# Kernel tuning notes

Measured on AMD Instinct MI355X. Metric: run time of the kernel, lower is better.

Reference implementation:

```python
import jax, jax.numpy as jnp
import numpy as np

N_NODES = 100000
N_EDGES = 3200000
D_IN = 256
D_OUT = 128


def setup_inputs() -> dict:
    key = jax.random.key(0)
    k1, k2, k3, k4, k5 = jax.random.split(key, 5)
    x = jax.random.normal(k1, (N_NODES, D_IN), dtype=jnp.float32)
    edge_src = jax.random.randint(k2, (N_EDGES,), 0, N_NODES, dtype=jnp.int32)
    edge_dst = jax.random.randint(k3, (N_EDGES,), 0, N_NODES, dtype=jnp.int32)
    edge_weight = jax.random.uniform(k4, (N_EDGES,), dtype=jnp.float32)
    # GraphConvolution weight init: uniform(-stdv, stdv), stdv = 1/sqrt(in+out)
    stdv = 1.0 / np.sqrt(D_IN + D_OUT)
    W = jax.random.uniform(k5, (D_IN, D_OUT), dtype=jnp.float32,
                           minval=-stdv, maxval=stdv)
    return {"x": x, "edge_src": edge_src, "edge_dst": edge_dst,
            "edge_weight": edge_weight, "W": W}


def reference(x, edge_src, edge_dst, edge_weight, W):
    # support = input @ weight  (dense GEMM)  [N, D_OUT]
    support = x @ W
    # out = spmm(adj, support): out[d] = sum_{e: dst(e)=d} w_e * support[src(e)]
    msgs = support[edge_src] * edge_weight[:, None]       # [E, D_OUT] gather
    out = jax.ops.segment_sum(msgs, edge_dst, num_segments=N_NODES)  # scatter-add
    return out
```

## Files before the change

### kernel.cpp

```cpp
#include <hip/hip_runtime.h>


#define DIN 256
#define DOUT 128
#define SB_SHIFT 10
#define SB_NODES 1024
#define MAX_NSB 128
#define TILE 4096
#define SPLIT 2

__device__ __forceinline__ unsigned pack_bf16x2(float a, float b) {
  unsigned ua = __float_as_uint(a);
  unsigned ub = __float_as_uint(b);
  ua += 0x7fffu + ((ua >> 16) & 1u);
  ub += 0x7fffu + ((ub >> 16) & 1u);
  return (ua >> 16) | (ub & 0xffff0000u);
}
__device__ __forceinline__ unsigned short bf16_rne(float a) {
  unsigned ua = __float_as_uint(a);
  ua += 0x7fffu + ((ua >> 16) & 1u);
  return (unsigned short)(ua >> 16);
}
__device__ __forceinline__ float bf_lo(unsigned p) { return __uint_as_float(p << 16); }
__device__ __forceinline__ float bf_hi(unsigned p) { return __uint_as_float(p & 0xffff0000u); }

typedef __attribute__((ext_vector_type(8))) short bf16x8;
typedef __attribute__((ext_vector_type(4))) float f32x4;

__global__ __launch_bounds__(256) void wtrans_kernel(const float* __restrict__ W,
                                                     unsigned short* __restrict__ Wt) {
  __shared__ float s[64][65];
  int t = threadIdx.x;
  int kt = blockIdx.x >> 1;
  int nt = blockIdx.x & 1;
#pragma unroll
  for (int i = 0; i < 16; i++) {
    int idx = i * 256 + t;
    int kk = idx >> 6, nn = idx & 63;
    s[kk][nn] = W[(size_t)(kt * 64 + kk) * DOUT + nt * 64 + nn];
  }
  __syncthreads();
#pragma unroll
  for (int i = 0; i < 16; i++) {
    int idx = i * 256 + t;
    int nn = idx >> 6, kk = idx & 63;
    Wt[(size_t)(nt * 64 + nn) * DIN + kt * 64 + kk] = bf16_rne(s[kk][nn]);
  }
}

__global__ __launch_bounds__(256) void gemm_mfma_kernel(const float* __restrict__ x,
                                                        const unsigned short* __restrict__ Wt,
                                                        unsigned short* __restrict__ support,
                                                        int M) {
  const int lane = threadIdx.x & 63;
  const int wave = threadIdx.x >> 6;
  const int m = lane & 15, kg = lane >> 4;
  const int rowBase = blockIdx.x * 128 + wave * 32;

  f32x4 acc[2][8];
#pragma unroll
  for (int rt = 0; rt < 2; rt++)
#pragma unroll
    for (int ct = 0; ct < 8; ct++) acc[rt][ct] = (f32x4)(0.f);

  const float* arow[2];
#pragma unroll
  for (int rt = 0; rt < 2; rt++) {
    int r = rowBase + rt * 16 + m;
    if (r > M - 1) r = M - 1;
    arow[rt] = x + (size_t)r * DIN + kg * 8;
  }
  const unsigned short* brow[8];
#pragma unroll
  for (int ct = 0; ct < 8; ct++)
    brow[ct] = Wt + (size_t)(ct * 16 + m) * DIN + kg * 8;

#pragma unroll 2
  for (int k0 = 0; k0 < DIN; k0 += 32) {
    bf16x8 af[2], bfr[8];
#pragma unroll
    for (int rt = 0; rt < 2; rt++) {
      float4 a0 = *(const float4*)(arow[rt] + k0);
      float4 a1 = *(const float4*)(arow[rt] + k0 + 4);
      union { bf16x8 f; unsigned u[4]; } ua;
      ua.u[0] = pack_bf16x2(a0.x, a0.y);
      ua.u[1] = pack_bf16x2(a0.z, a0.w);
      ua.u[2] = pack_bf16x2(a1.x, a1.y);
      ua.u[3] = pack_bf16x2(a1.z, a1.w);
      af[rt] = ua.f;
    }
#pragma unroll
    for (int ct = 0; ct < 8; ct++) {
      union { bf16x8 f; uint4 u; } ub;
      ub.u = *(const uint4*)(brow[ct] + k0);
      bfr[ct] = ub.f;
    }
#pragma unroll
    for (int rt = 0; rt < 2; rt++)
#pragma unroll
      for (int ct = 0; ct < 8; ct++)
        acc[rt][ct] = __builtin_amdgcn_mfma_f32_16x16x32_bf16(af[rt], bfr[ct],
                                                              acc[rt][ct], 0, 0, 0);
  }

#pragma unroll
  for (int rt = 0; rt < 2; rt++) {
#pragma unroll
    for (int r = 0; r < 4; r++) {
      int row = rowBase + rt * 16 + kg * 4 + r;
      if (row < M) {
#pragma unroll
        for (int ct = 0; ct < 8; ct++) {
          int col = ct * 16 + m;
          support[(size_t)row * DOUT + col] = bf16_rne(acc[rt][ct][r]);
        }
      }
    }
  }
}

__global__ __launch_bounds__(256) void sbhist_kernel(const int* __restrict__ dst, int E,
                                                     int nsb, int* __restrict__ sb_tot) {
  __shared__ int h[MAX_NSB];
  int t = threadIdx.x;
  for (int i = t; i < nsb; i += 256) h[i] = 0;
  __syncthreads();
  int e4 = E >> 2;
  for (int i = blockIdx.x * 256 + t; i < e4; i += gridDim.x * 256) {
    int4 d = *(const int4*)&dst[i * 4];
    atomicAdd(&h[d.x >> SB_SHIFT], 1);
    atomicAdd(&h[d.y >> SB_SHIFT], 1);
    atomicAdd(&h[d.z >> SB_SHIFT], 1);
    atomicAdd(&h[d.w >> SB_SHIFT], 1);
  }
  if (blockIdx.x == 0 && t < (E & 3)) atomicAdd(&h[dst[e4 * 4 + t] >> SB_SHIFT], 1);
  __syncthreads();
  for (int i = t; i < nsb; i += 256)
    if (h[i]) atomicAdd(&sb_tot[i], h[i]);
}

__global__ __launch_bounds__(128) void sbscan_kernel(const int* __restrict__ sb_tot, int nsb,
                                                     int* __restrict__ sb_base,
                                                     int* __restrict__ sb_cur) {
  __shared__ int s[128];
  int t = threadIdx.x;
  int v = (t < nsb) ? sb_tot[t] : 0;
  s[t] = v;
  __syncthreads();
  for (int off = 1; off < 128; off <<= 1) {
    int u = (t >= off) ? s[t - off] : 0;
    __syncthreads();
    s[t] += u;
    __syncthreads();
  }
  if (t < nsb) {
    int excl = s[t] - v;
    sb_base[t] = excl;
    sb_cur[t] = excl;
  }
}

__global__ __launch_bounds__(256) void bin1_kernel(const int* __restrict__ src,
                                                   const int* __restrict__ dst,
                                                   const float* __restrict__ w,
                                                   int E, int nsb,
                                                   int* __restrict__ sb_cur,
                                                   uint2* __restrict__ bin) {
  __shared__ uint2 recs[TILE];
  __shared__ unsigned short sbid[TILE];
  __shared__ int hist[MAX_NSB], segstart[MAX_NSB], cursor[MAX_NSB], sbbase[MAX_NSB];
  __shared__ int sc[128];
  int t = threadIdx.x;
  int e0 = blockIdx.x * TILE;
  int cnt = min(TILE, E - e0);

  for (int i = t; i < nsb; i += 256) hist[i] = 0;
  __syncthreads();
  for (int k = 0; k < TILE / 256; k++) {
    int e = e0 + k * 256 + t;
    if (e < E) atomicAdd(&hist[dst[e] >> SB_SHIFT], 1);
  }
  __syncthreads();
  if (t < 128) sc[t] = (t < nsb) ? hist[t] : 0;
  __syncthreads();
  for (int off = 1; off < 128; off <<= 1) {
    int v = 0;
    if (t < 128 && t >= off) v = sc[t - off];
    __syncthreads();
    if (t < 128) sc[t] += v;
    __syncthreads();
  }
  if (t < nsb) {
    int c = hist[t];
    int excl = sc[t] - c;
    segstart[t] = excl;
    cursor[t] = excl;
    if (c > 0) sbbase[t] = atomicAdd(&sb_cur[t], c);
  }
  __syncthreads();
  for (int k = 0; k < TILE / 256; k++) {
    int e = e0 + k * 256 + t;
    if (e < E) {
      int d = dst[e];
      int sb = d >> SB_SHIFT;
      int slot = atomicAdd(&cursor[sb], 1);
      recs[slot] = make_uint2((unsigned)src[e] | ((unsigned)(d & (SB_NODES - 1)) << 17),
                              __float_as_uint(w[e]));
      sbid[slot] = (unsigned short)sb;
    }
  }
  __syncthreads();
  for (int k = 0; k < TILE / 256; k++) {
    int slot = k * 256 + t;
    if (slot < cnt) {
      int sb = sbid[slot];
      bin[sbbase[sb] + (slot - segstart[sb])] = recs[slot];
    }
  }
}

__global__ __launch_bounds__(256) void bin2_kernel(const uint2* __restrict__ bin,
                                                   const int* __restrict__ sb_base,
                                                   const int* __restrict__ sb_cur,
                                                   int N, int E,
                                                   int* __restrict__ row_ptr,
                                                   unsigned* __restrict__ csr) {
  __shared__ int lhist[SB_NODES];
  __shared__ int part[256];
  int t = threadIdx.x;
  int sb = blockIdx.x / SPLIT;
  int q = blockIdx.x % SPLIT;
  int nodeBase = sb * SB_NODES;
  int beg = sb_base[sb];
  int end = sb_cur[sb];

  for (int i = t; i < SB_NODES; i += 256) lhist[i] = 0;
  __syncthreads();
  for (int i = beg + t; i < end; i += 256) {
    uint2 r = bin[i];
    atomicAdd(&lhist[(r.x >> 17) & (SB_NODES - 1)], 1);
  }
  __syncthreads();
  int a0 = lhist[4 * t], a1 = lhist[4 * t + 1], a2 = lhist[4 * t + 2], a3 = lhist[4 * t + 3];
  int tsum = a0 + a1 + a2 + a3;
  part[t] = tsum;
  __syncthreads();
  for (int off = 1; off < 256; off <<= 1) {
    int v = (t >= off) ? part[t - off] : 0;
    __syncthreads();
    part[t] += v;
    __syncthreads();
  }
  int excl = part[t] - tsum;
  lhist[4 * t] = excl;
  lhist[4 * t + 1] = excl + a0;
  lhist[4 * t + 2] = excl + a0 + a1;
  lhist[4 * t + 3] = excl + a0 + a1 + a2;
  __syncthreads();
  if (q == 0) {
    for (int l = t; l < SB_NODES; l += 256) {
      int node = nodeBase + l;
      if (node < N) row_ptr[node] = beg + lhist[l];
    }
    if (t == 0 && nodeBase + SB_NODES >= N) row_ptr[N] = E;
  }
  __syncthreads();
  int lo = q * (SB_NODES / SPLIT);
  int hi = lo + (SB_NODES / SPLIT);
  for (int i = beg + t; i < end; i += 256) {
    uint2 r = bin[i];
    int local = (int)((r.x >> 17) & (SB_NODES - 1));
    if (local >= lo && local < hi) {
      int pos = beg + atomicAdd(&lhist[local], 1);
      float wf = __uint_as_float(r.y);
      unsigned wq = (unsigned)(wf * 32767.f + 0.5f);
      if (wq > 32767u) wq = 32767u;
      csr[pos] = (r.x & 0x1FFFFu) | (wq << 17);
    }
  }
}

__global__ __launch_bounds__(256) void spmm_kernel(const unsigned* __restrict__ sup,
                                                   const int* __restrict__ row_ptr,
                                                   const unsigned* __restrict__ csr,
                                                   float* __restrict__ out, int N,
                                                   int pass) {
  int wave = threadIdx.x >> 6;
  int lane = threadIdx.x & 63;
  int g = lane >> 4;
  int c = lane & 15;
  int node = blockIdx.x * 4 + wave;
  if (node >= N) return;
  int j0 = row_ptr[node];
  int j1 = row_ptr[node + 1];
  const unsigned* supb = sup + pass * 32 + c * 2;
  float acc[4] = {0.f, 0.f, 0.f, 0.f};
  const float wscale = 1.f / 32767.f;

  for (int base = j0; base < j1; base += 64) {
    int cnt = min(64, j1 - base);
    unsigned myrec = 0;
    if (lane < cnt) myrec = csr[base + lane];
    for (int j = 0; j < cnt; j += 16) {
      uint2 p[4];
      float wv[4];
#pragma unroll
      for (int u = 0; u < 4; u++) {
        int e = j + 4 * u + g;
        int jj = min(e, cnt - 1);
        unsigned r = (unsigned)__shfl((int)myrec, jj, 64);
        int s = (int)(r & 0x1FFFFu);
        float ww = (float)(r >> 17) * wscale;
        wv[u] = (e < cnt) ? ww : 0.f;
        p[u] = *(const uint2*)(supb + (size_t)s * 64);
      }
#pragma unroll
      for (int u = 0; u < 4; u++) {
        acc[0] += wv[u] * bf_lo(p[u].x);
        acc[1] += wv[u] * bf_hi(p[u].x);
        acc[2] += wv[u] * bf_lo(p[u].y);
        acc[3] += wv[u] * bf_hi(p[u].y);
      }
    }
  }
#pragma unroll
  for (int i = 0; i < 4; i++) {
    acc[i] += __shfl_xor(acc[i], 16, 64);
    acc[i] += __shfl_xor(acc[i], 32, 64);
  }
  if (g == 0) {
    float* orow = out + (size_t)node * DOUT + pass * 64 + c * 4;
    *(float4*)orow = make_float4(acc[0], acc[1], acc[2], acc[3]);
  }
}

__global__ void scatter_kernel(const float* __restrict__ x, const float* __restrict__ W,
                               const int* __restrict__ src, const int* __restrict__ dst,
                               const float* __restrict__ w, long long total,
                               float* __restrict__ out) {
  long long i = (long long)blockIdx.x * blockDim.x + threadIdx.x;
  if (i < total) {
    int e = (int)(i >> 7);
    int c = (int)(i & 127);
    float acc = 0.f;
    const float* xr = &x[(size_t)src[e] * DIN];
    for (int k = 0; k < DIN; k++) acc += xr[k] * W[(size_t)k * DOUT + c];
    atomicAdd(&out[(size_t)dst[e] * DOUT + c], w[e] * acc);
  }
}

extern "C" void kernel_launch(void* const* d_in, const int* in_sizes, int n_in,
                              void* d_out, int out_size, void* d_ws, size_t ws_size,
                              hipStream_t stream) {
  const float* x = (const float*)d_in[0];
  const int* esrc = (const int*)d_in[1];
  const int* edst = (const int*)d_in[2];
  const float* ew = (const float*)d_in[3];
  const float* W = (const float*)d_in[4];
  float* out = (float*)d_out;

  const int N = in_sizes[0] / DIN;
  const int E = in_sizes[1];
  const int nsb = (N + SB_NODES - 1) / SB_NODES;

  char* ws = (char*)d_ws;
  size_t off = 0;
  auto alloc = [&](size_t bytes) {
    size_t o = off;
    off = (off + bytes + 255) & ~(size_t)255;
    return o;
  };
  size_t sup_off = alloc((size_t)N * DOUT * 2);
  size_t wt_off = alloc((size_t)DOUT * DIN * 2);
  size_t rp_off = alloc((size_t)(N + 1) * 4);
  size_t sbt_off = alloc(MAX_NSB * 4);
  size_t sbb_off = alloc(MAX_NSB * 4);
  size_t sbc_off = alloc(MAX_NSB * 4);
  size_t bin_off = alloc((size_t)E * 8);
  size_t csr_off = alloc((size_t)E * 4);
  bool use_csr = (off <= ws_size);

  unsigned short* support = (unsigned short*)(ws + sup_off);
  unsigned short* Wt = (unsigned short*)(ws + wt_off);
  int* row_ptr = (int*)(ws + rp_off);
  int* sb_tot = (int*)(ws + sbt_off);
  int* sb_base = (int*)(ws + sbb_off);
  int* sb_cur = (int*)(ws + sbc_off);
  uint2* bin = (uint2*)(ws + bin_off);
  unsigned* csr = (unsigned*)(ws + csr_off);

  if (use_csr) {
    wtrans_kernel<<<8, 256, 0, stream>>>(W, Wt);
    gemm_mfma_kernel<<<(N + 127) / 128, 256, 0, stream>>>(x, Wt, support, N);
    hipMemsetAsync(sb_tot, 0, MAX_NSB * 4, stream);
    sbhist_kernel<<<512, 256, 0, stream>>>(edst, E, nsb, sb_tot);
    sbscan_kernel<<<1, 128, 0, stream>>>(sb_tot, nsb, sb_base, sb_cur);
    bin1_kernel<<<(E + TILE - 1) / TILE, 256, 0, stream>>>(esrc, edst, ew, E, nsb,
                                                           sb_cur, bin);
    bin2_kernel<<<nsb * SPLIT, 256, 0, stream>>>(bin, sb_base, sb_cur, N, E,
                                                 row_ptr, csr);
    spmm_kernel<<<(N + 3) / 4, 256, 0, stream>>>((const unsigned*)support, row_ptr, csr,
                                                 out, N, 0);
    spmm_kernel<<<(N + 3) / 4, 256, 0, stream>>>((const unsigned*)support, row_ptr, csr,
                                                 out, N, 1);
  } else {
    hipMemsetAsync(out, 0, (size_t)N * DOUT * 4, stream);
    long long total = (long long)E * DOUT;
    scatter_kernel<<<(int)((total + 255) / 256), 256, 0, stream>>>(x, W, esrc, edst, ew,
                                                                   total, out);
  }
}
```

Measured before the change: 478.6 us.

## Compute per-node degrees globally and replace bin2 with parallel global-atomic scatter

After: 676.3 us. 1.41x slower.

```diff
diff --git a/kernel.cpp b/kernel.cpp
--- a/kernel.cpp
+++ b/kernel.cpp
@@ -7,7 +7,7 @@
 #define SB_NODES 1024
 #define MAX_NSB 128
 #define TILE 4096
-#define SPLIT 2
+#define RSPLIT 8
 
 __device__ __forceinline__ unsigned pack_bf16x2(float a, float b) {
   unsigned ua = __float_as_uint(a);
@@ -120,7 +120,8 @@
 }
 
 __global__ __launch_bounds__(256) void sbhist_kernel(const int* __restrict__ dst, int E,
-                                                     int nsb, int* __restrict__ sb_tot) {
+                                                     int nsb, int* __restrict__ sb_tot,
+                                                     int* __restrict__ deg) {
   __shared__ int h[MAX_NSB];
   int t = threadIdx.x;
   for (int i = t; i < nsb; i += 256) h[i] = 0;
@@ -132,8 +133,16 @@
     atomicAdd(&h[d.y >> SB_SHIFT], 1);
     atomicAdd(&h[d.z >> SB_SHIFT], 1);
     atomicAdd(&h[d.w >> SB_SHIFT], 1);
-  }
-  if (blockIdx.x == 0 && t < (E & 3)) atomicAdd(&h[dst[e4 * 4 + t] >> SB_SHIFT], 1);
+    atomicAdd(&deg[d.x], 1);
+    atomicAdd(&deg[d.y], 1);
+    atomicAdd(&deg[d.z], 1);
+    atomicAdd(&deg[d.w], 1);
+  }
+  if (blockIdx.x == 0 && t < (E & 3)) {
+    int d = dst[e4 * 4 + t];
+    atomicAdd(&h[d >> SB_SHIFT], 1);
+    atomicAdd(&deg[d], 1);
+  }
   __syncthreads();
   for (int i = t; i < nsb; i += 256)
     if (h[i]) atomicAdd(&sb_tot[i], h[i]);
@@ -158,6 +167,44 @@
     sb_base[t] = excl;
     sb_cur[t] = excl;
   }
+}
+
+__global__ __launch_bounds__(256) void rowscan_kernel(const int* __restrict__ deg,
+                                                      const int* __restrict__ sb_base,
+                                                      int N, int E,
+                                                      int* __restrict__ row_ptr,
+                                                      int* __restrict__ row_cur) {
+  __shared__ int part[256];
+  int sb = blockIdx.x;
+  int t = threadIdx.x;
+  int nodeBase = sb * SB_NODES;
+  int d[4];
+  int tsum = 0;
+#pragma unroll
+  for (int u = 0; u < 4; u++) {
+    int node = nodeBase + 4 * t + u;
+    d[u] = (node < N) ? deg[node] : 0;
+    tsum += d[u];
+  }
+  part[t] = tsum;
+  __syncthreads();
+  for (int off = 1; off < 256; off <<= 1) {
+    int v = (t >= off) ? part[t - off] : 0;
+    __syncthreads();
+    part[t] += v;
+    __syncthreads();
+  }
+  int excl = sb_base[sb] + part[t] - tsum;
+#pragma unroll
+  for (int u = 0; u < 4; u++) {
+    int node = nodeBase + 4 * t + u;
+    if (node < N) {
+      row_ptr[node] = excl;
+      row_cur[node] = excl;
+    }
+    excl += d[u];
+  }
+  if (sb == gridDim.x - 1 && t == 0) row_ptr[N] = E;
 }
 
 __global__ __launch_bounds__(256) void bin1_kernel(const int* __restrict__ src,
@@ -219,64 +266,27 @@
   }
 }
 
-__global__ __launch_bounds__(256) void bin2_kernel(const uint2* __restrict__ bin,
-                                                   const int* __restrict__ sb_base,
-                                                   const int* __restrict__ sb_cur,
-                                                   int N, int E,
-                                                   int* __restrict__ row_ptr,
-                                                   unsigned* __restrict__ csr) {
-  __shared__ int lhist[SB_NODES];
-  __shared__ int part[256];
-  int t = threadIdx.x;
-  int sb = blockIdx.x / SPLIT;
-  int q = blockIdx.x % SPLIT;
-  int nodeBase = sb * SB_NODES;
+__global__ __launch_bounds__(256) void scatter2_kernel(const uint2* __restrict__ bin,
+                                                       const int* __restrict__ sb_base,
+                                                       const int* __restrict__ sb_tot,
+                                                       int* __restrict__ row_cur,
+                                                       unsigned* __restrict__ csr) {
+  int sb = blockIdx.x / RSPLIT;
+  int q = blockIdx.x % RSPLIT;
   int beg = sb_base[sb];
-  int end = sb_cur[sb];
-
-  for (int i = t; i < SB_NODES; i += 256) lhist[i] = 0;
-  __syncthreads();
-  for (int i = beg + t; i < end; i += 256) {
+  int len = sb_tot[sb];
+  int per = (len + RSPLIT - 1) / RSPLIT;
+  int lo = beg + q * per;
+  int hi = beg + min(len, (q + 1) * per);
+  int nodeBase = sb << SB_SHIFT;
+  for (int i = lo + threadIdx.x; i < hi; i += 256) {
     uint2 r = bin[i];
-    atomicAdd(&lhist[(r.x >> 17) & (SB_NODES - 1)], 1);
-  }
-  __syncthreads();
-  int a0 = lhist[4 * t], a1 = lhist[4 * t + 1], a2 = lhist[4 * t + 2], a3 = lhist[4 * t + 3];
-  int tsum = a0 + a1 + a2 + a3;
-  part[t] = tsum;
-  __syncthreads();
-  for (int off = 1; off < 256; off <<= 1) {
-    int v = (t >= off) ? part[t - off] : 0;
-    __syncthreads();
-    part[t] += v;
-    __syncthreads();
-  }
-  int excl = part[t] - tsum;
-  lhist[4 * t] = excl;
-  lhist[4 * t + 1] = excl + a0;
-  lhist[4 * t + 2] = excl + a0 + a1;
-  lhist[4 * t + 3] = excl + a0 + a1 + a2;
-  __syncthreads();
-  if (q == 0) {
-    for (int l = t; l < SB_NODES; l += 256) {
-      int node = nodeBase + l;
-      if (node < N) row_ptr[node] = beg + lhist[l];
-    }
-    if (t == 0 && nodeBase + SB_NODES >= N) row_ptr[N] = E;
-  }
-  __syncthreads();
-  int lo = q * (SB_NODES / SPLIT);
-  int hi = lo + (SB_NODES / SPLIT);
-  for (int i = beg + t; i < end; i += 256) {
-    uint2 r = bin[i];
-    int local = (int)((r.x >> 17) & (SB_NODES - 1));
-    if (local >= lo && local < hi) {
-      int pos = beg + atomicAdd(&lhist[local], 1);
-      float wf = __uint_as_float(r.y);
-      unsigned wq = (unsigned)(wf * 32767.f + 0.5f);
-      if (wq > 32767u) wq = 32767u;
-      csr[pos] = (r.x & 0x1FFFFu) | (wq << 17);
-    }
+    int node = nodeBase + (int)((r.x >> 17) & (SB_NODES - 1));
+    int pos = atomicAdd(&row_cur[node], 1);
+    float wf = __uint_as_float(r.y);
+    unsigned wq = (unsigned)(wf * 32767.f + 0.5f);
+    if (wq > 32767u) wq = 32767u;
+    csr[pos] = (r.x & 0x1FFFFu) | (wq << 17);
   }
 }
 
@@ -373,6 +383,8 @@
   size_t sup_off = alloc((size_t)N * DOUT * 2);
   size_t wt_off = alloc((size_t)DOUT * DIN * 2);
   size_t rp_off = alloc((size_t)(N + 1) * 4);
+  size_t deg_off = alloc((size_t)N * 4);
+  size_t rcur_off = alloc((size_t)N * 4);
   size_t sbt_off = alloc(MAX_NSB * 4);
   size_t sbb_off = alloc(MAX_NSB * 4);
   size_t sbc_off = alloc(MAX_NSB * 4);
@@ -383,6 +395,8 @@
   unsigned short* support = (unsigned short*)(ws + sup_off);
   unsigned short* Wt = (unsigned short*)(ws + wt_off);
   int* row_ptr = (int*)(ws + rp_off);
+  int* deg = (int*)(ws + deg_off);
+  int* row_cur = (int*)(ws + rcur_off);
   int* sb_tot = (int*)(ws + sbt_off);
   int* sb_base = (int*)(ws + sbb_off);
   int* sb_cur = (int*)(ws + sbc_off);
@@ -393,12 +407,14 @@
     wtrans_kernel<<<8, 256, 0, stream>>>(W, Wt);
     gemm_mfma_kernel<<<(N + 127) / 128, 256, 0, stream>>>(x, Wt, support, N);
     hipMemsetAsync(sb_tot, 0, MAX_NSB * 4, stream);
-    sbhist_kernel<<<512, 256, 0, stream>>>(edst, E, nsb, sb_tot);
+    hipMemsetAsync(deg, 0, (size_t)N * 4, stream);
+    sbhist_kernel<<<512, 256, 0, stream>>>(edst, E, nsb, sb_tot, deg);
     sbscan_kernel<<<1, 128, 0, stream>>>(sb_tot, nsb, sb_base, sb_cur);
+    rowscan_kernel<<<nsb, 256, 0, stream>>>(deg, sb_base, N, E, row_ptr, row_cur);
     bin1_kernel<<<(E + TILE - 1) / TILE, 256, 0, stream>>>(esrc, edst, ew, E, nsb,
                                                            sb_cur, bin);
-    bin2_kernel<<<nsb * SPLIT, 256, 0, stream>>>(bin, sb_base, sb_cur, N, E,
-                                                 row_ptr, csr);
+    scatter2_kernel<<<nsb * RSPLIT, 256, 0, stream>>>(bin, sb_base, sb_tot,
+                                                      row_cur, csr);
     spmm_kernel<<<(N + 3) / 4, 256, 0, stream>>>((const unsigned*)support, row_ptr, csr,
                                                  out, N, 0);
     spmm_kernel<<<(N + 3) / 4, 256, 0, stream>>>((const unsigned*)support, row_ptr, csr,
```

## Split second binning pass into chunked histogram, scan and scatter kernels

Applied to the files above, without the earlier changes.

New measurement: 412.0 us. -13.9%, faster.

```diff
diff --git a/kernel.cpp b/kernel.cpp
--- a/kernel.cpp
+++ b/kernel.cpp
@@ -7,7 +7,7 @@
 #define SB_NODES 1024
 #define MAX_NSB 128
 #define TILE 4096
-#define SPLIT 2
+#define CH 8
 
 __device__ __forceinline__ unsigned pack_bf16x2(float a, float b) {
   unsigned ua = __float_as_uint(a);
@@ -165,8 +165,10 @@
                                                    const float* __restrict__ w,
                                                    int E, int nsb,
                                                    int* __restrict__ sb_cur,
-                                                   uint2* __restrict__ bin) {
-  __shared__ uint2 recs[TILE];
+                                                   unsigned* __restrict__ binq,
+                                                   unsigned short* __restrict__ binl) {
+  __shared__ unsigned lq[TILE];
+  __shared__ unsigned short ll[TILE];
   __shared__ unsigned short sbid[TILE];
   __shared__ int hist[MAX_NSB], segstart[MAX_NSB], cursor[MAX_NSB], sbbase[MAX_NSB];
   __shared__ int sc[128];
@@ -204,8 +206,11 @@
       int d = dst[e];
       int sb = d >> SB_SHIFT;
       int slot = atomicAdd(&cursor[sb], 1);
-      recs[slot] = make_uint2((unsigned)src[e] | ((unsigned)(d & (SB_NODES - 1)) << 17),
-                              __float_as_uint(w[e]));
+      float wf = w[e];
+      unsigned wq = (unsigned)(wf * 32767.f + 0.5f);
+      if (wq > 32767u) wq = 32767u;
+      lq[slot] = (unsigned)src[e] | (wq << 17);
+      ll[slot] = (unsigned short)(d & (SB_NODES - 1));
       sbid[slot] = (unsigned short)sb;
     }
   }
@@ -214,35 +219,63 @@
     int slot = k * 256 + t;
     if (slot < cnt) {
       int sb = sbid[slot];
-      bin[sbbase[sb] + (slot - segstart[sb])] = recs[slot];
-    }
-  }
-}
-
-__global__ __launch_bounds__(256) void bin2_kernel(const uint2* __restrict__ bin,
-                                                   const int* __restrict__ sb_base,
-                                                   const int* __restrict__ sb_cur,
-                                                   int N, int E,
-                                                   int* __restrict__ row_ptr,
-                                                   unsigned* __restrict__ csr) {
-  __shared__ int lhist[SB_NODES];
+      int p = sbbase[sb] + (slot - segstart[sb]);
+      binq[p] = lq[slot];
+      binl[p] = ll[slot];
+    }
+  }
+}
+
+__device__ __forceinline__ bool sb_chunk(int g, int nsb, int nsb8, int& sb, int& c) {
+  int xcd = g & 7;
+  int i = g >> 3;
+  sb = xcd + 8 * (i % nsb8);
+  c = i / nsb8;
+  return sb < nsb;
+}
+
+__global__ __launch_bounds__(256) void histC_kernel(const unsigned short* __restrict__ binl,
+                                                    const int* __restrict__ sb_base,
+                                                    const int* __restrict__ sb_tot,
+                                                    int nsb, int nsb8,
+                                                    int* __restrict__ chist) {
+  __shared__ int h[SB_NODES];
+  int sb, c;
+  if (!sb_chunk(blockIdx.x, nsb, nsb8, sb, c)) return;
+  int t = threadIdx.x;
+  for (int l = t; l < SB_NODES; l += 256) h[l] = 0;
+  __syncthreads();
+  int beg = sb_base[sb], len = sb_tot[sb];
+  int per = (len + CH - 1) / CH;
+  int lo = beg + min(len, c * per);
+  int hi = beg + min(len, (c + 1) * per);
+  for (int e = lo + t; e < hi; e += 256)
+    atomicAdd(&h[binl[e]], 1);
+  __syncthreads();
+  int* dstp = chist + ((size_t)sb * CH + c) * SB_NODES;
+  for (int l = t; l < SB_NODES; l += 256) dstp[l] = h[l];
+}
+
+__global__ __launch_bounds__(256) void rowscanC_kernel(int* __restrict__ chist,
+                                                       const int* __restrict__ sb_base,
+                                                       int N, int E, int nsb,
+                                                       int* __restrict__ row_ptr) {
   __shared__ int part[256];
-  int t = threadIdx.x;
-  int sb = blockIdx.x / SPLIT;
-  int q = blockIdx.x % SPLIT;
-  int nodeBase = sb * SB_NODES;
-  int beg = sb_base[sb];
-  int end = sb_cur[sb];
-
-  for (int i = t; i < SB_NODES; i += 256) lhist[i] = 0;
-  __syncthreads();
-  for (int i = beg + t; i < end; i += 256) {
-    uint2 r = bin[i];
-    atomicAdd(&lhist[(r.x >> 17) & (SB_NODES - 1)], 1);
-  }
-  __syncthreads();
-  int a0 = lhist[4 * t], a1 = lhist[4 * t + 1], a2 = lhist[4 * t + 2], a3 = lhist[4 * t + 3];
-  int tsum = a0 + a1 + a2 + a3;
+  int sb = blockIdx.x;
+  int t = threadIdx.x;
+  int* base = chist + (size_t)sb * CH * SB_NODES;
+  int cnt[4][CH];
+  int tsum = 0;
+#pragma unroll
+  for (int u = 0; u < 4; u++) {
+    int l = 4 * t + u;
+#pragma unroll
+    for (int c = 0; c < CH; c++) {
+      int v = base[c * SB_NODES + l];
+      cnt[u][c] = v;
+      tsum += v;
+    }
+  }
   part[t] = tsum;
   __syncthreads();
   for (int off = 1; off < 256; off <<= 1) {
@@ -251,32 +284,44 @@
     part[t] += v;
     __syncthreads();
   }
-  int excl = part[t] - tsum;
-  lhist[4 * t] = excl;
-  lhist[4 * t + 1] = excl + a0;
-  lhist[4 * t + 2] = excl + a0 + a1;
-  lhist[4 * t + 3] = excl + a0 + a1 + a2;
-  __syncthreads();
-  if (q == 0) {
-    for (int l = t; l < SB_NODES; l += 256) {
-      int node = nodeBase + l;
-      if (node < N) row_ptr[node] = beg + lhist[l];
-    }
-    if (t == 0 && nodeBase + SB_NODES >= N) row_ptr[N] = E;
-  }
-  __syncthreads();
-  int lo = q * (SB_NODES / SPLIT);
-  int hi = lo + (SB_NODES / SPLIT);
-  for (int i = beg + t; i < end; i += 256) {
-    uint2 r = bin[i];
-    int local = (int)((r.x >> 17) & (SB_NODES - 1));
-    if (local >= lo && local < hi) {
-      int pos = beg + atomicAdd(&lhist[local], 1);
-      float wf = __uint_as_float(r.y);
-      unsigned wq = (unsigned)(wf * 32767.f + 0.5f);
-      if (wq > 32767u) wq = 32767u;
-      csr[pos] = (r.x & 0x1FFFFu) | (wq << 17);
-    }
+  int run = sb_base[sb] + part[t] - tsum;
+  int nodeBase = sb << SB_SHIFT;
+#pragma unroll
+  for (int u = 0; u < 4; u++) {
+    int l = 4 * t + u;
+    int node = nodeBase + l;
+    if (node < N) row_ptr[node] = run;
+#pragma unroll
+    for (int c = 0; c < CH; c++) {
+      base[c * SB_NODES + l] = run;
+      run += cnt[u][c];
+    }
+  }
+  if (sb == nsb - 1 && t == 0) row_ptr[N] = E;
+}
+
+__global__ __launch_bounds__(256) void scatterC_kernel(const unsigned* __restrict__ binq,
+                                                       const unsigned short* __restrict__ binl,
+                                                       const int* __restrict__ sb_base,
+                                                       const int* __restrict__ sb_tot,
+                                                       const int* __restrict__ chist,
+                                                       int nsb, int nsb8,
+                                                       unsigned* __restrict__ csr) {
+  __shared__ int cur[SB_NODES];
+  int sb, c;
+  if (!sb_chunk(blockIdx.x, nsb, nsb8, sb, c)) return;
+  int t = threadIdx.x;
+  const int* cb = chist + ((size_t)sb * CH + c) * SB_NODES;
+  for (int l = t; l < SB_NODES; l += 256) cur[l] = cb[l];
+  __syncthreads();
+  int beg = sb_base[sb], len = sb_tot[sb];
+  int per = (len + CH - 1) / CH;
+  int lo = beg + min(len, c * per);
+  int hi = beg + min(len, (c + 1) * per);
+  for (int e = lo + t; e < hi; e += 256) {
+    int l = binl[e];
+    int pos = atomicAdd(&cur[l], 1);
+    csr[pos] = binq[e];
   }
 }
 
@@ -362,6 +407,7 @@
   const int N = in_sizes[0] / DIN;
   const int E = in_sizes[1];
   const int nsb = (N + SB_NODES - 1) / SB_NODES;
+  const int nsb8 = (nsb + 7) / 8;
 
   char* ws = (char*)d_ws;
   size_t off = 0;
@@ -376,7 +422,9 @@
   size_t sbt_off = alloc(MAX_NSB * 4);
   size_t sbb_off = alloc(MAX_NSB * 4);
   size_t sbc_off = alloc(MAX_NSB * 4);
-  size_t bin_off = alloc((size_t)E * 8);
+  size_t binq_off = alloc((size_t)E * 4);
+  size_t binl_off = alloc((size_t)E * 2);
+  size_t chist_off = alloc((size_t)nsb * CH * SB_NODES * 4);
   size_t csr_off = alloc((size_t)E * 4);
   bool use_csr = (off <= ws_size);
 
@@ -386,7 +434,9 @@
   int* sb_tot = (int*)(ws + sbt_off);
   int* sb_base = (int*)(ws + sbb_off);
   int* sb_cur = (int*)(ws + sbc_off);
-  uint2* bin = (uint2*)(ws + bin_off);
+  unsigned* binq = (unsigned*)(ws + binq_off);
+  unsigned short* binl = (unsigned short*)(ws + binl_off);
+  int* chist = (int*)(ws + chist_off);
   unsigned* csr = (unsigned*)(ws + csr_off);
 
   if (use_csr) {
@@ -396,9 +446,12 @@
     sbhist_kernel<<<512, 256, 0, stream>>>(edst, E, nsb, sb_tot);
     sbscan_kernel<<<1, 128, 0, stream>>>(sb_tot, nsb, sb_base, sb_cur);
     bin1_kernel<<<(E + TILE - 1) / TILE, 256, 0, stream>>>(esrc, edst, ew, E, nsb,
-                                                           sb_cur, bin);
-    bin2_kernel<<<nsb * SPLIT, 256, 0, stream>>>(bin, sb_base, sb_cur, N, E,
-                                                 row_ptr, csr);
+                                                           sb_cur, binq, binl);
+    histC_kernel<<<8 * nsb8 * CH, 256, 0, stream>>>(binl, sb_base, sb_tot, nsb, nsb8,
+                                                    chist);
+    rowscanC_kernel<<<nsb, 256, 0, stream>>>(chist, sb_base, N, E, nsb, row_ptr);
+    scatterC_kernel<<<8 * nsb8 * CH, 256, 0, stream>>>(binq, binl, sb_base, sb_tot,
+                                                       chist, nsb, nsb8, csr);
     spmm_kernel<<<(N + 3) / 4, 256, 0, stream>>>((const unsigned*)support, row_ptr, csr,
                                                  out, N, 0);
     spmm_kernel<<<(N + 3) / 4, 256, 0, stream>>>((const unsigned*)support, row_ptr, csr,
```
